# Performance work log

Hardware: AMD Instinct MI355X
Metric: run time of the kernel (lower is better)

The kernel has to match this reference:

```python
import jax, jax.numpy as jnp
import numpy as np

N, E, H, D, F_IN = 50000, 400000, 2, 128, 5
EPS = 1e-5  # BatchNorm eps

def _bn(x, gamma, beta, rm, rv):
    # eval-mode BatchNorm1d using running stats
    return (x - rm) * jax.lax.rsqrt(rv + EPS) * gamma + beta

def setup_inputs() -> dict:
    key = jax.random.key(0)
    ks = jax.random.split(key, 24)
    r = lambda i, shape, s=1.0: jax.random.normal(ks[i], shape, jnp.float32) * s
    u = lambda i, shape: jax.random.uniform(ks[i], shape, jnp.float32)
    return {
        "h": r(0, (N, F_IN)),
        "edge_index": jax.random.randint(ks[1], (2, E), 0, N),
        "edge_weight": r(2, (E, 1)),
        # BatchNorm1d(5)
        "gamma1": 1.0 + r(3, (F_IN,), 0.1), "beta1": r(4, (F_IN,), 0.1),
        "rm1": r(5, (F_IN,), 0.1), "rv1": 0.5 + u(6, (F_IN,)),
        # GATv2Conv params (lin_l, lin_r with bias; lin_edge no bias; att; out bias)
        "Wl": r(7, (F_IN, H * D), 0.2), "bl": r(8, (H * D,), 0.1),
        "Wr": r(9, (F_IN, H * D), 0.2), "br": r(10, (H * D,), 0.1),
        "We": r(11, (1, H * D), 0.2),
        "att": r(12, (H, D), 0.2),
        "bias_gat": r(13, (D,), 0.1),
        # fc1 + BatchNorm1d(128)
        "W1": r(14, (D, D), 0.08), "b1": r(15, (D,), 0.1),
        "gamma2": 1.0 + r(16, (D,), 0.1), "beta2": r(17, (D,), 0.1),
        "rm2": r(18, (D,), 0.1), "rv2": 0.5 + u(19, (D,)),
        # fc2
        "W2": r(20, (D, F_IN), 0.08), "b2": r(21, (F_IN,), 0.1),
    }

def reference(h, edge_index, edge_weight, gamma1, beta1, rm1, rv1,
              Wl, bl, Wr, br, We, att, bias_gat,
              W1, b1, gamma2, beta2, rm2, rv2, W2, b2):
    src, dst = edge_index[0], edge_index[1]
    h = _bn(h, gamma1, beta1, rm1, rv1)
    xl = (h @ Wl + bl).reshape(N, H, D)   # source transform (messages)
    xr = (h @ Wr + br).reshape(N, H, D)   # destination transform
    e = (edge_weight @ We).reshape(E, H, D)
    # GATv2: score = att . leaky_relu(x_j + x_i + edge_emb), slope 0.2
    z = jax.nn.leaky_relu(xl[src] + xr[dst] + e, 0.2)          # [E,H,D]
    logits = jnp.einsum('ehd,hd->eh', z, att)                   # [E,H]
    # segment softmax over edges sharing a destination node
    mx = jax.ops.segment_max(logits, dst, num_segments=N)       # [N,H]
    ex = jnp.exp(logits - mx[dst])
    den = jax.ops.segment_sum(ex, dst, num_segments=N)
    alpha = ex / (den[dst] + 1e-16)                             # [E,H]
    msg = xl[src] * alpha[:, :, None]                           # [E,H,D]
    ssum = jax.ops.segment_sum(msg, dst, num_segments=N)        # [N,H,D]
    cnt = jax.ops.segment_sum(jnp.ones((E,), jnp.float32), dst, num_segments=N)
    out = ssum / jnp.maximum(cnt, 1.0)[:, None, None]           # aggr='mean'
    out = out.mean(axis=1) + bias_gat                           # concat=False -> head mean
    out = out @ W1 + b1
    out = _bn(out, gamma2, beta2, rm2, rv2)
    out = jax.nn.leaky_relu(out, 0.01)
    # dropout is identity in eval mode
    out = out @ W2 + b2                                         # [N,5]
    return out
```

## Files before the change

kernel.cpp:

```cpp
#include <hip/hip_runtime.h>

#define N_NODES 50000
#define N_EDGES 400000
#define F_INP 5
#define HD 256
#define BN_EPS 1e-5f

typedef short v8s __attribute__((ext_vector_type(8)));
typedef float v4f __attribute__((ext_vector_type(4)));
typedef unsigned v4u __attribute__((ext_vector_type(4)));

#define OFF_HBN  0
#define OFF_ACC  400000
#define OFF_BPK  1200000
#define OFF_WF   1202048
#define OFF_W2P  1204096

#define PREP_BLOCKS 3125

#define DPP_ROR_F(x, n) \
    __int_as_float(__builtin_amdgcn_update_dpp(0, __float_as_int(x), 0x120 | (n), 0xF, 0xF, false))

__device__ __forceinline__ unsigned short f2bf(float f) {
    unsigned u = __float_as_uint(f);
    return (unsigned short)((u + 0x7FFFu + ((u >> 16) & 1u)) >> 16);
}
__device__ __forceinline__ unsigned pk2(float a, float b) {
    return (unsigned)f2bf(a) | ((unsigned)f2bf(b) << 16);
}

__device__ __forceinline__ float wcat(int k, int c, const float* Wl, const float* Wr,
                                      const float* We, const float* bl, const float* br) {
    if (k < 5)   return Wl[k * HD + c];
    if (k < 10)  return Wr[(k - 5) * HD + c];
    if (k == 10) return We[c];
    return bl[c] + br[c];
}

__global__ void k_prep(const float* __restrict__ h, const float* __restrict__ g1,
                       const float* __restrict__ be1, const float* __restrict__ rm1,
                       const float* __restrict__ rv1,
                       const float* __restrict__ Wl, const float* __restrict__ bl,
                       const float* __restrict__ Wr, const float* __restrict__ br,
                       const float* __restrict__ We, const float* __restrict__ att,
                       const float* __restrict__ bias_gat,
                       const float* __restrict__ W1, const float* __restrict__ b1,
                       const float* __restrict__ g2, const float* __restrict__ be2,
                       const float* __restrict__ rm2, const float* __restrict__ rv2,
                       const float* __restrict__ W2,
                       float* __restrict__ hbn8, float* __restrict__ acc,
                       unsigned* __restrict__ Bpk,
                       float* __restrict__ Wf, float* __restrict__ W2p) {
    if (blockIdx.x < PREP_BLOCKS) {
        int i = blockIdx.x * blockDim.x + threadIdx.x;
        if (i < N_NODES * 16) acc[i] = 0.f;
        if (i < N_NODES * 8) {
            int f = i & 7, n = i >> 3;
            float v = 0.f;
            if (f < F_INP) {
                float x = h[n * F_INP + f];
                v = (x - rm1[f]) * rsqrtf(rv1[f] + BN_EPS) * g1[f] + be1[f];
            }
            hbn8[i] = v;
        }
        if (i < 1024) {
            int t = i >> 6, l = i & 63;
            int g = l >> 4, c = t * 16 + (l & 15);
            unsigned d0 = 0, d1 = 0;
            if (g < 3) {
                int kb = 4 * g;
                d0 = pk2(wcat(kb + 0, c, Wl, Wr, We, bl, br),
                         wcat(kb + 1, c, Wl, Wr, We, bl, br));
                d1 = pk2(wcat(kb + 2, c, Wl, Wr, We, bl, br),
                         wcat(kb + 3, c, Wl, Wr, We, bl, br));
            }
            Bpk[(t * 64 + l) * 2 + 0] = d0;
            Bpk[(t * 64 + l) * 2 + 1] = d1;
        }
        return;
    }
    int k = blockIdx.x - PREP_BLOCKS;
    int c = threadIdx.x;
    if (c >= 128) return;
    const float* base = (k == 0) ? bl
                      : (k == 1) ? bl + 128
                      : (k < 7)  ? Wl + (k - 2) * HD
                      : (k < 12) ? Wl + (k - 7) * HD + 128
                                 : bias_gat;
    float sum = 0.f;
#pragma unroll 8
    for (int d = 0; d < 128; ++d) sum += base[d] * W1[d * 128 + c];
    if (k == 12) sum += b1[c];
    Wf[c * 16 + k] = sum;
    if (k == 0) {
        float sc = g2[c] * rsqrtf(rv2[c] + BN_EPS);
        Wf[c * 16 + 13] = sc;
        Wf[c * 16 + 14] = be2[c] - rm2[c] * sc;
        Wf[c * 16 + 15] = 0.f;
#pragma unroll
        for (int f = 0; f < 8; ++f)
            W2p[c * 8 + f] = (f < 5) ? W2[c * 5 + f] : 0.f;
    }
}

__launch_bounds__(256)
__global__ void k_edge(const float* __restrict__ hbn8, const int* __restrict__ ei,
                       const float* __restrict__ ew, const unsigned* __restrict__ Bpk,
                       const float* __restrict__ att, float* __restrict__ acc) {
    int lane = threadIdx.x & 63;
    int wv = threadIdx.x >> 6;
    int g = lane >> 4, e16 = lane & 15;

    v8s B[16];
    float AT[16];
#pragma unroll
    for (int t = 0; t < 16; ++t) {
        uint2 d = *(const uint2*)&Bpk[(t * 64 + lane) * 2];
        v4u u = {d.x, d.y, 0u, 0u};
        B[t] = __builtin_bit_cast(v8s, u);
        AT[t] = att[t * 16 + e16];
    }

    int wid = blockIdx.x * 4 + wv;
    int nw = gridDim.x * 4;
    const int NT = N_EDGES / 16;

    int j16 = e16;
    bool sact = j16 < 13;
    int kk = (j16 < 6) ? j16 - 1 : j16 - 7;
    int kc = min(max(kk, 0), 4);

    for (int tile = wid; tile < NT; tile += nw) {
        int e = tile * 16 + e16;
        int src = ei[e];
        int dst = ei[N_EDGES + e];
        float w = ew[e];
        float4 s4 = *(const float4*)&hbn8[src * 8];
        float hs4 = hbn8[src * 8 + 4];
        float4 d4 = *(const float4*)&hbn8[dst * 8];
        float hd4 = hbn8[dst * 8 + 4];

        float a0 = (g == 0) ? s4.x : (g == 1) ? hs4  : d4.w;
        float a1 = (g == 0) ? s4.y : (g == 1) ? d4.x : hd4;
        float a2 = (g == 0) ? s4.z : (g == 1) ? d4.y : w;
        float a3 = (g == 0) ? s4.w : (g == 1) ? d4.z : 1.0f;
        unsigned ua0 = (g < 3) ? pk2(a0, a1) : 0u;
        unsigned ua1 = (g < 3) ? pk2(a2, a3) : 0u;
        v4u uav = {ua0, ua1, 0u, 0u};
        v8s A = __builtin_bit_cast(v8s, uav);

        float p00 = 0.f, p01 = 0.f, p02 = 0.f, p03 = 0.f;
        float p10 = 0.f, p11 = 0.f, p12 = 0.f, p13v = 0.f;
        v4f zero = {0.f, 0.f, 0.f, 0.f};
#pragma unroll
        for (int t = 0; t < 8; ++t) {
            v4f c = __builtin_amdgcn_mfma_f32_16x16x32_bf16(A, B[t], zero, 0, 0, 0);
            p00 += AT[t] * fmaf(0.66666667f, fabsf(c[0]), c[0]);
            p01 += AT[t] * fmaf(0.66666667f, fabsf(c[1]), c[1]);
            p02 += AT[t] * fmaf(0.66666667f, fabsf(c[2]), c[2]);
            p03 += AT[t] * fmaf(0.66666667f, fabsf(c[3]), c[3]);
        }
#pragma unroll
        for (int t = 8; t < 16; ++t) {
            v4f c = __builtin_amdgcn_mfma_f32_16x16x32_bf16(A, B[t], zero, 0, 0, 0);
            p10 += AT[t] * fmaf(0.66666667f, fabsf(c[0]), c[0]);
            p11 += AT[t] * fmaf(0.66666667f, fabsf(c[1]), c[1]);
            p12 += AT[t] * fmaf(0.66666667f, fabsf(c[2]), c[2]);
            p13v += AT[t] * fmaf(0.66666667f, fabsf(c[3]), c[3]);
        }
#pragma unroll
        for (int st = 1; st <= 8; st <<= 1) {
            if (st == 1) {
                p00 += DPP_ROR_F(p00, 1); p01 += DPP_ROR_F(p01, 1);
                p02 += DPP_ROR_F(p02, 1); p03 += DPP_ROR_F(p03, 1);
                p10 += DPP_ROR_F(p10, 1); p11 += DPP_ROR_F(p11, 1);
                p12 += DPP_ROR_F(p12, 1); p13v += DPP_ROR_F(p13v, 1);
            } else if (st == 2) {
                p00 += DPP_ROR_F(p00, 2); p01 += DPP_ROR_F(p01, 2);
                p02 += DPP_ROR_F(p02, 2); p03 += DPP_ROR_F(p03, 2);
                p10 += DPP_ROR_F(p10, 2); p11 += DPP_ROR_F(p11, 2);
                p12 += DPP_ROR_F(p12, 2); p13v += DPP_ROR_F(p13v, 2);
            } else if (st == 4) {
                p00 += DPP_ROR_F(p00, 4); p01 += DPP_ROR_F(p01, 4);
                p02 += DPP_ROR_F(p02, 4); p03 += DPP_ROR_F(p03, 4);
                p10 += DPP_ROR_F(p10, 4); p11 += DPP_ROR_F(p11, 4);
                p12 += DPP_ROR_F(p12, 4); p13v += DPP_ROR_F(p13v, 4);
            } else {
                p00 += DPP_ROR_F(p00, 8); p01 += DPP_ROR_F(p01, 8);
                p02 += DPP_ROR_F(p02, 8); p03 += DPP_ROR_F(p03, 8);
                p10 += DPP_ROR_F(p10, 8); p11 += DPP_ROR_F(p11, 8);
                p12 += DPP_ROR_F(p12, 8); p13v += DPP_ROR_F(p13v, 8);
            }
        }
        float e00 = __expf(0.6f * p00), e01 = __expf(0.6f * p01);
        float e02 = __expf(0.6f * p02), e03 = __expf(0.6f * p03);
        float e10 = __expf(0.6f * p10), e11 = __expf(0.6f * p11);
        float e12 = __expf(0.6f * p12), e13 = __expf(0.6f * p13v);

        if (sact) {
#pragma unroll
            for (int it = 0; it < 4; ++it) {
                int eg = tile * 16 + 4 * g + it;
                int srcg = ei[eg];
                int deg = ei[N_EDGES + eg];
                float hsel = hbn8[srcg * 8 + kc];
                float ex0 = (it == 0) ? e00 : (it == 1) ? e01 : (it == 2) ? e02 : e03;
                float ex1 = (it == 0) ? e10 : (it == 1) ? e11 : (it == 2) ? e12 : e13;
                float base = (j16 < 6) ? ex0 : ex1;
                float v = base * hsel;
                v = (j16 == 0) ? ex0 : v;
                v = (j16 == 6) ? ex1 : v;
                v = (j16 == 12) ? 1.0f : v;
                atomicAdd(&acc[deg * 16 + j16], v);
            }
        }
    }
}

__launch_bounds__(256)
__global__ void k_mlp(const float* __restrict__ acc, const float* __restrict__ Wf,
                      const float* __restrict__ W2p, const float* __restrict__ b2,
                      float* __restrict__ out) {
    int n = blockIdx.x * blockDim.x + threadIdx.x;
    if (n >= N_NODES) return;
    const float* ar = acc + (size_t)n * 16;
    float4 A0 = *(const float4*)(ar + 0);
    float4 A1 = *(const float4*)(ar + 4);
    float4 A2 = *(const float4*)(ar + 8);
    float cnt = ar[12];
    float r0 = 1.f / (A0.x + 1e-16f);
    float r1 = 1.f / (A1.z + 1e-16f);
    float scale = 0.5f / fmaxf(cnt, 1.f);
    float s0 = scale * r0, s1 = scale * r1;
    float m0 = A0.x * s0, m1 = A1.z * s1;
    float m2 = A0.y * s0, m3 = A0.z * s0, m4 = A0.w * s0, m5 = A1.x * s0, m6 = A1.y * s0;
    float m7 = A1.w * s1, m8 = A2.x * s1, m9 = A2.y * s1, m10 = A2.z * s1, m11 = A2.w * s1;

    float o0 = 0.f, o1 = 0.f, o2 = 0.f, o3 = 0.f, o4 = 0.f;
#pragma unroll 4
    for (int c = 0; c < 128; ++c) {
        const float* wr = &Wf[c * 16];
        float a = wr[12];
        a += m0 * wr[0] + m1 * wr[1] + m2 * wr[2] + m3 * wr[3];
        a += m4 * wr[4] + m5 * wr[5] + m6 * wr[6] + m7 * wr[7];
        a += m8 * wr[8] + m9 * wr[9] + m10 * wr[10] + m11 * wr[11];
        a = fmaf(a, wr[13], wr[14]);
        a = fmaxf(a, 0.01f * a);
        const float* w2 = &W2p[c * 8];
        o0 = fmaf(a, w2[0], o0);
        o1 = fmaf(a, w2[1], o1);
        o2 = fmaf(a, w2[2], o2);
        o3 = fmaf(a, w2[3], o3);
        o4 = fmaf(a, w2[4], o4);
    }
    float* op = out + (size_t)n * 5;
    op[0] = o0 + b2[0];
    op[1] = o1 + b2[1];
    op[2] = o2 + b2[2];
    op[3] = o3 + b2[3];
    op[4] = o4 + b2[4];
}

extern "C" void kernel_launch(void* const* d_in, const int* in_sizes, int n_in,
                              void* d_out, int out_size, void* d_ws, size_t ws_size,
                              hipStream_t stream) {
    const float* h    = (const float*)d_in[0];
    const int*   ei   = (const int*)d_in[1];
    const float* ew   = (const float*)d_in[2];
    const float* g1   = (const float*)d_in[3];
    const float* be1  = (const float*)d_in[4];
    const float* rm1  = (const float*)d_in[5];
    const float* rv1  = (const float*)d_in[6];
    const float* Wl   = (const float*)d_in[7];
    const float* bl   = (const float*)d_in[8];
    const float* Wr   = (const float*)d_in[9];
    const float* br   = (const float*)d_in[10];
    const float* We   = (const float*)d_in[11];
    const float* att  = (const float*)d_in[12];
    const float* bias_gat = (const float*)d_in[13];
    const float* W1   = (const float*)d_in[14];
    const float* b1   = (const float*)d_in[15];
    const float* g2   = (const float*)d_in[16];
    const float* be2  = (const float*)d_in[17];
    const float* rm2  = (const float*)d_in[18];
    const float* rv2  = (const float*)d_in[19];
    const float* W2   = (const float*)d_in[20];
    const float* b2   = (const float*)d_in[21];

    float* ws  = (float*)d_ws;
    float* hbn = ws + OFF_HBN;
    float* acc = ws + OFF_ACC;
    unsigned* Bpk = (unsigned*)(ws + OFF_BPK);
    float* Wf  = ws + OFF_WF;
    float* W2p = ws + OFF_W2P;

    k_prep<<<PREP_BLOCKS + 13, 256, 0, stream>>>(
        h, g1, be1, rm1, rv1, Wl, bl, Wr, br, We, att, bias_gat,
        W1, b1, g2, be2, rm2, rv2, W2, hbn, acc, Bpk, Wf, W2p);
    k_edge<<<1280, 256, 0, stream>>>(hbn, ei, ew, Bpk, att, acc);
    k_mlp<<<(N_NODES + 255) / 256, 256, 0, stream>>>(acc, Wf, W2p, b2, (float*)d_out);
}
```

Before: 87.57 us.

## Split weight folding into own kernel and parallelize MLP across 8 lanes per node

Weight folding (W1 contractions) moves out of k_prep into a separate k_fold kernel, and each fold block now splits its 128-long dot product across four thread groups that combine through shared memory. k_mlp now assigns 8 threads per node, each covering 16 hidden channels with vectorized float4 weight loads, and reduces the partial outputs with shuffles. This shortens the serial 128-iteration loop per thread. The edge grid drops from 1280 to 1024 blocks and the DPP reduction loop is written out by hand. The extra kernel launch adds a little overhead.

Result: slower. 128.8 us (+47.1%).

```diff
diff --git a/kernel.cpp b/kernel.cpp
--- a/kernel.cpp
+++ b/kernel.cpp
@@ -17,6 +17,7 @@
 #define OFF_W2P  1204096
 
 #define PREP_BLOCKS 3125
+#define NT_ALL   25000
 
 #define DPP_ROR_F(x, n) \
     __int_as_float(__builtin_amdgcn_update_dpp(0, __float_as_int(x), 0x120 | (n), 0xF, 0xF, false))
@@ -43,63 +44,73 @@
                        const float* __restrict__ Wl, const float* __restrict__ bl,
                        const float* __restrict__ Wr, const float* __restrict__ br,
                        const float* __restrict__ We, const float* __restrict__ att,
+                       float* __restrict__ hbn8, float* __restrict__ acc,
+                       unsigned* __restrict__ Bpk) {
+    int i = blockIdx.x * blockDim.x + threadIdx.x;
+    if (i < N_NODES * 16) acc[i] = 0.f;
+    if (i < N_NODES * 8) {
+        int f = i & 7, n = i >> 3;
+        float v = 0.f;
+        if (f < F_INP) {
+            float x = h[n * F_INP + f];
+            v = (x - rm1[f]) * rsqrtf(rv1[f] + BN_EPS) * g1[f] + be1[f];
+        }
+        hbn8[i] = v;
+    }
+    if (i < 1024) {
+        int t = i >> 6, l = i & 63;
+        int g = l >> 4, c = t * 16 + (l & 15);
+        unsigned d0 = 0, d1 = 0;
+        if (g < 3) {
+            int kb = 4 * g;
+            d0 = pk2(wcat(kb + 0, c, Wl, Wr, We, bl, br),
+                     wcat(kb + 1, c, Wl, Wr, We, bl, br));
+            d1 = pk2(wcat(kb + 2, c, Wl, Wr, We, bl, br),
+                     wcat(kb + 3, c, Wl, Wr, We, bl, br));
+        }
+        Bpk[(t * 64 + l) * 2 + 0] = d0;
+        Bpk[(t * 64 + l) * 2 + 1] = d1;
+    }
+}
+
+__global__ void k_fold(const float* __restrict__ Wl, const float* __restrict__ bl,
                        const float* __restrict__ bias_gat,
                        const float* __restrict__ W1, const float* __restrict__ b1,
                        const float* __restrict__ g2, const float* __restrict__ be2,
                        const float* __restrict__ rm2, const float* __restrict__ rv2,
                        const float* __restrict__ W2,
-                       float* __restrict__ hbn8, float* __restrict__ acc,
-                       unsigned* __restrict__ Bpk,
                        float* __restrict__ Wf, float* __restrict__ W2p) {
-    if (blockIdx.x < PREP_BLOCKS) {
-        int i = blockIdx.x * blockDim.x + threadIdx.x;
-        if (i < N_NODES * 16) acc[i] = 0.f;
-        if (i < N_NODES * 8) {
-            int f = i & 7, n = i >> 3;
-            float v = 0.f;
-            if (f < F_INP) {
-                float x = h[n * F_INP + f];
-                v = (x - rm1[f]) * rsqrtf(rv1[f] + BN_EPS) * g1[f] + be1[f];
-            }
-            hbn8[i] = v;
-        }
-        if (i < 1024) {
-            int t = i >> 6, l = i & 63;
-            int g = l >> 4, c = t * 16 + (l & 15);
-            unsigned d0 = 0, d1 = 0;
-            if (g < 3) {
-                int kb = 4 * g;
-                d0 = pk2(wcat(kb + 0, c, Wl, Wr, We, bl, br),
-                         wcat(kb + 1, c, Wl, Wr, We, bl, br));
-                d1 = pk2(wcat(kb + 2, c, Wl, Wr, We, bl, br),
-                         wcat(kb + 3, c, Wl, Wr, We, bl, br));
-            }
-            Bpk[(t * 64 + l) * 2 + 0] = d0;
-            Bpk[(t * 64 + l) * 2 + 1] = d1;
-        }
-        return;
-    }
-    int k = blockIdx.x - PREP_BLOCKS;
-    int c = threadIdx.x;
-    if (c >= 128) return;
+    __shared__ float part[4][128];
+    int k = blockIdx.x;
+    int c = threadIdx.x & 127;
+    int q = threadIdx.x >> 7;
     const float* base = (k == 0) ? bl
                       : (k == 1) ? bl + 128
                       : (k < 7)  ? Wl + (k - 2) * HD
                       : (k < 12) ? Wl + (k - 7) * HD + 128
                                  : bias_gat;
-    float sum = 0.f;
-#pragma unroll 8
-    for (int d = 0; d < 128; ++d) sum += base[d] * W1[d * 128 + c];
-    if (k == 12) sum += b1[c];
-    Wf[c * 16 + k] = sum;
-    if (k == 0) {
-        float sc = g2[c] * rsqrtf(rv2[c] + BN_EPS);
-        Wf[c * 16 + 13] = sc;
-        Wf[c * 16 + 14] = be2[c] - rm2[c] * sc;
-        Wf[c * 16 + 15] = 0.f;
-#pragma unroll
-        for (int f = 0; f < 8; ++f)
-            W2p[c * 8 + f] = (f < 5) ? W2[c * 5 + f] : 0.f;
+    float s0 = 0.f, s1 = 0.f;
+    int d0 = 32 * q;
+#pragma unroll
+    for (int d = 0; d < 32; d += 2) {
+        s0 += base[d0 + d]     * W1[(d0 + d) * 128 + c];
+        s1 += base[d0 + d + 1] * W1[(d0 + d + 1) * 128 + c];
+    }
+    part[q][c] = s0 + s1;
+    __syncthreads();
+    if (q == 0) {
+        float sum = part[0][c] + part[1][c] + part[2][c] + part[3][c];
+        if (k == 12) sum += b1[c];
+        Wf[c * 16 + k] = sum;
+        if (k == 0) {
+            float sc = g2[c] * rsqrtf(rv2[c] + BN_EPS);
+            Wf[c * 16 + 13] = sc;
+            Wf[c * 16 + 14] = be2[c] - rm2[c] * sc;
+            Wf[c * 16 + 15] = 0.f;
+#pragma unroll
+            for (int f = 0; f < 8; ++f)
+                W2p[c * 8 + f] = (f < 5) ? W2[c * 5 + f] : 0.f;
+        }
     }
 }
 
@@ -123,14 +134,13 @@
 
     int wid = blockIdx.x * 4 + wv;
     int nw = gridDim.x * 4;
-    const int NT = N_EDGES / 16;
 
     int j16 = e16;
     bool sact = j16 < 13;
     int kk = (j16 < 6) ? j16 - 1 : j16 - 7;
     int kc = min(max(kk, 0), 4);
 
-    for (int tile = wid; tile < NT; tile += nw) {
+    for (int tile = wid; tile < NT_ALL; tile += nw) {
         int e = tile * 16 + e16;
         int src = ei[e];
         int dst = ei[N_EDGES + e];
@@ -168,30 +178,23 @@
             p12 += AT[t] * fmaf(0.66666667f, fabsf(c[2]), c[2]);
             p13v += AT[t] * fmaf(0.66666667f, fabsf(c[3]), c[3]);
         }
-#pragma unroll
-        for (int st = 1; st <= 8; st <<= 1) {
-            if (st == 1) {
-                p00 += DPP_ROR_F(p00, 1); p01 += DPP_ROR_F(p01, 1);
-                p02 += DPP_ROR_F(p02, 1); p03 += DPP_ROR_F(p03, 1);
-                p10 += DPP_ROR_F(p10, 1); p11 += DPP_ROR_F(p11, 1);
-                p12 += DPP_ROR_F(p12, 1); p13v += DPP_ROR_F(p13v, 1);
-            } else if (st == 2) {
-                p00 += DPP_ROR_F(p00, 2); p01 += DPP_ROR_F(p01, 2);
-                p02 += DPP_ROR_F(p02, 2); p03 += DPP_ROR_F(p03, 2);
-                p10 += DPP_ROR_F(p10, 2); p11 += DPP_ROR_F(p11, 2);
-                p12 += DPP_ROR_F(p12, 2); p13v += DPP_ROR_F(p13v, 2);
-            } else if (st == 4) {
-                p00 += DPP_ROR_F(p00, 4); p01 += DPP_ROR_F(p01, 4);
-                p02 += DPP_ROR_F(p02, 4); p03 += DPP_ROR_F(p03, 4);
-                p10 += DPP_ROR_F(p10, 4); p11 += DPP_ROR_F(p11, 4);
-                p12 += DPP_ROR_F(p12, 4); p13v += DPP_ROR_F(p13v, 4);
-            } else {
-                p00 += DPP_ROR_F(p00, 8); p01 += DPP_ROR_F(p01, 8);
-                p02 += DPP_ROR_F(p02, 8); p03 += DPP_ROR_F(p03, 8);
-                p10 += DPP_ROR_F(p10, 8); p11 += DPP_ROR_F(p11, 8);
-                p12 += DPP_ROR_F(p12, 8); p13v += DPP_ROR_F(p13v, 8);
-            }
-        }
+        p00 += DPP_ROR_F(p00, 1); p01 += DPP_ROR_F(p01, 1);
+        p02 += DPP_ROR_F(p02, 1); p03 += DPP_ROR_F(p03, 1);
+        p10 += DPP_ROR_F(p10, 1); p11 += DPP_ROR_F(p11, 1);
+        p12 += DPP_ROR_F(p12, 1); p13v += DPP_ROR_F(p13v, 1);
+        p00 += DPP_ROR_F(p00, 2); p01 += DPP_ROR_F(p01, 2);
+        p02 += DPP_ROR_F(p02, 2); p03 += DPP_ROR_F(p03, 2);
+        p10 += DPP_ROR_F(p10, 2); p11 += DPP_ROR_F(p11, 2);
+        p12 += DPP_ROR_F(p12, 2); p13v += DPP_ROR_F(p13v, 2);
+        p00 += DPP_ROR_F(p00, 4); p01 += DPP_ROR_F(p01, 4);
+        p02 += DPP_ROR_F(p02, 4); p03 += DPP_ROR_F(p03, 4);
+        p10 += DPP_ROR_F(p10, 4); p11 += DPP_ROR_F(p11, 4);
+        p12 += DPP_ROR_F(p12, 4); p13v += DPP_ROR_F(p13v, 4);
+        p00 += DPP_ROR_F(p00, 8); p01 += DPP_ROR_F(p01, 8);
+        p02 += DPP_ROR_F(p02, 8); p03 += DPP_ROR_F(p03, 8);
+        p10 += DPP_ROR_F(p10, 8); p11 += DPP_ROR_F(p11, 8);
+        p12 += DPP_ROR_F(p12, 8); p13v += DPP_ROR_F(p13v, 8);
+
         float e00 = __expf(0.6f * p00), e01 = __expf(0.6f * p01);
         float e02 = __expf(0.6f * p02), e03 = __expf(0.6f * p03);
         float e10 = __expf(0.6f * p10), e11 = __expf(0.6f * p11);
@@ -221,7 +224,9 @@
 __global__ void k_mlp(const float* __restrict__ acc, const float* __restrict__ Wf,
                       const float* __restrict__ W2p, const float* __restrict__ b2,
                       float* __restrict__ out) {
-    int n = blockIdx.x * blockDim.x + threadIdx.x;
+    int t = blockIdx.x * blockDim.x + threadIdx.x;
+    int n = t >> 3;
+    int q = t & 7;
     if (n >= N_NODES) return;
     const float* ar = acc + (size_t)n * 16;
     float4 A0 = *(const float4*)(ar + 0);
@@ -237,28 +242,45 @@
     float m7 = A1.w * s1, m8 = A2.x * s1, m9 = A2.y * s1, m10 = A2.z * s1, m11 = A2.w * s1;
 
     float o0 = 0.f, o1 = 0.f, o2 = 0.f, o3 = 0.f, o4 = 0.f;
+    int cbase = q * 16;
 #pragma unroll 4
-    for (int c = 0; c < 128; ++c) {
-        const float* wr = &Wf[c * 16];
-        float a = wr[12];
-        a += m0 * wr[0] + m1 * wr[1] + m2 * wr[2] + m3 * wr[3];
-        a += m4 * wr[4] + m5 * wr[5] + m6 * wr[6] + m7 * wr[7];
-        a += m8 * wr[8] + m9 * wr[9] + m10 * wr[10] + m11 * wr[11];
-        a = fmaf(a, wr[13], wr[14]);
+    for (int i = 0; i < 16; ++i) {
+        const float* wr = &Wf[(cbase + i) * 16];
+        float4 w0 = *(const float4*)(wr + 0);
+        float4 w1 = *(const float4*)(wr + 4);
+        float4 w2v = *(const float4*)(wr + 8);
+        float4 w3 = *(const float4*)(wr + 12);
+        float a = w3.x;
+        a += m0 * w0.x + m1 * w0.y + m2 * w0.z + m3 * w0.w;
+        a += m4 * w1.x + m5 * w1.y + m6 * w1.z + m7 * w1.w;
+        a += m8 * w2v.x + m9 * w2v.y + m10 * w2v.z + m11 * w2v.w;
+        a = fmaf(a, w3.y, w3.z);
         a = fmaxf(a, 0.01f * a);
-        const float* w2 = &W2p[c * 8];
-        o0 = fmaf(a, w2[0], o0);
-        o1 = fmaf(a, w2[1], o1);
-        o2 = fmaf(a, w2[2], o2);
-        o3 = fmaf(a, w2[3], o3);
-        o4 = fmaf(a, w2[4], o4);
-    }
-    float* op = out + (size_t)n * 5;
-    op[0] = o0 + b2[0];
-    op[1] = o1 + b2[1];
-    op[2] = o2 + b2[2];
-    op[3] = o3 + b2[3];
-    op[4] = o4 + b2[4];
+        const float* w2 = &W2p[(cbase + i) * 8];
+        float4 wa = *(const float4*)w2;
+        float wb = w2[4];
+        o0 = fmaf(a, wa.x, o0);
+        o1 = fmaf(a, wa.y, o1);
+        o2 = fmaf(a, wa.z, o2);
+        o3 = fmaf(a, wa.w, o3);
+        o4 = fmaf(a, wb, o4);
+    }
+#pragma unroll
+    for (int m = 1; m <= 4; m <<= 1) {
+        o0 += __shfl_xor(o0, m);
+        o1 += __shfl_xor(o1, m);
+        o2 += __shfl_xor(o2, m);
+        o3 += __shfl_xor(o3, m);
+        o4 += __shfl_xor(o4, m);
+    }
+    if (q == 0) {
+        float* op = out + (size_t)n * 5;
+        op[0] = o0 + b2[0];
+        op[1] = o1 + b2[1];
+        op[2] = o2 + b2[2];
+        op[3] = o3 + b2[3];
+        op[4] = o4 + b2[4];
+    }
 }
 
 extern "C" void kernel_launch(void* const* d_in, const int* in_sizes, int n_in,
@@ -294,9 +316,11 @@
     float* Wf  = ws + OFF_WF;
     float* W2p = ws + OFF_W2P;
 
-    k_prep<<<PREP_BLOCKS + 13, 256, 0, stream>>>(
-        h, g1, be1, rm1, rv1, Wl, bl, Wr, br, We, att, bias_gat,
-        W1, b1, g2, be2, rm2, rv2, W2, hbn, acc, Bpk, Wf, W2p);
-    k_edge<<<1280, 256, 0, stream>>>(hbn, ei, ew, Bpk, att, acc);
-    k_mlp<<<(N_NODES + 255) / 256, 256, 0, stream>>>(acc, Wf, W2p, b2, (float*)d_out);
-}
+    k_prep<<<PREP_BLOCKS, 256, 0, stream>>>(
+        h, g1, be1, rm1, rv1, Wl, bl, Wr, br, We, att, hbn, acc, Bpk);
+    k_fold<<<13, 512, 0, stream>>>(Wl, bl, bias_gat, W1, b1, g2, be2, rm2, rv2, W2,
+                                   Wf, W2p);
+    k_edge<<<1024, 256, 0, stream>>>(hbn, ei, ew, Bpk, att, acc);
+    k_mlp<<<(N_NODES * 8 + 255) / 256, 256, 0, stream>>>(acc, Wf, W2p, b2,
+                                                         (float*)d_out);
+}
```
